# Kernel tuning notes

Measured on AMD Instinct MI355X. Metric: run time of the kernel, lower is better.

## Reference

```python
import jax, jax.numpy as jnp
import numpy as np

EMBED = 256; HEADS = 8; LEVELS = 1; POINTS = 4; QUEUE = 2
HB = 200; WB = 200; NQ = HB * WB; BS = 1


def bilinear_sample(img, grid, h, w):
    # img: (BH, D, h*w) flattened feature map; grid: (BH, N, 2) in [-1, 1]
    # torch.grid_sample(align_corners=False, padding_mode='zeros') semantics
    gx, gy = grid[..., 0], grid[..., 1]
    x = (gx + 1.0) * (w * 0.5) - 0.5
    y = (gy + 1.0) * (h * 0.5) - 0.5
    x0 = jnp.floor(x); y0 = jnp.floor(y)
    lx = x - x0; ly = y - y0
    x0i = x0.astype(jnp.int32); y0i = y0.astype(jnp.int32)

    def corner(xi, yi, wgt):
        valid = ((xi >= 0) & (xi < w) & (yi >= 0) & (yi < h)).astype(img.dtype)
        idx = jnp.clip(yi, 0, h - 1) * w + jnp.clip(xi, 0, w - 1)  # (BH, N)
        vals = jax.vmap(lambda im, ix: im[:, ix])(img, idx)  # (BH, D, N)
        return vals * (wgt * valid)[:, None, :]

    return (corner(x0i, y0i, (1 - lx) * (1 - ly))
            + corner(x0i + 1, y0i, lx * (1 - ly))
            + corner(x0i, y0i + 1, (1 - lx) * ly)
            + corner(x0i + 1, y0i + 1, lx * ly))


def ms_deform_attn(value, shapes, loc, aw):
    # value: (B, Nv, H, D); loc: (B, nq, H, L, P, 2); aw: (B, nq, H, L, P)
    B, Nv, H, D = value.shape
    nq = loc.shape[1]; P = loc.shape[4]
    grids = 2.0 * loc - 1.0
    start = 0
    per_level = []
    for l in range(shapes.shape[0]):
        h, w = int(shapes[l, 0]), int(shapes[l, 1])
        vl = value[:, start:start + h * w].reshape(B, h, w, H, D)
        vl = vl.transpose(0, 3, 4, 1, 2).reshape(B * H, D, h * w)
        g = grids[:, :, :, l].transpose(0, 2, 1, 3, 4).reshape(B * H, nq * P, 2)
        samp = bilinear_sample(vl, g, h, w).reshape(B, H, D, nq, P)
        per_level.append(samp)
        start += h * w
    sampled = jnp.stack(per_level, axis=4)  # (B, H, D, nq, L, P)
    w_ = aw.transpose(0, 2, 1, 3, 4)[:, :, None]  # (B, H, 1, nq, L, P)
    out = (sampled * w_).sum(axis=(-1, -2))  # (B, H, D, nq)
    return out.reshape(B, H * D, nq).transpose(0, 2, 1)  # (B, nq, E)


def setup_inputs():
    key = jax.random.key(0)
    ks = jax.random.split(key, 10)
    s = 0.02
    n_off = QUEUE * HEADS * LEVELS * POINTS * 2
    n_aw = QUEUE * HEADS * LEVELS * POINTS
    return {
        "query": jax.random.normal(ks[0], (BS, NQ, EMBED), jnp.float32),
        "query_pos": jax.random.normal(ks[1], (BS, NQ, EMBED), jnp.float32),
        "value": jax.random.normal(ks[2], (BS * QUEUE, NQ, EMBED), jnp.float32),
        "reference_points": jax.random.uniform(ks[3], (BS * QUEUE, NQ, LEVELS, 2), jnp.float32),
        "spatial_shapes": jnp.array([[HB, WB]], dtype=jnp.int32),
        "W_off": jax.random.normal(ks[4], (EMBED * QUEUE, n_off), jnp.float32) * s,
        "b_off": jnp.zeros((n_off,), jnp.float32),
        "W_attn": jax.random.normal(ks[5], (EMBED * QUEUE, n_aw), jnp.float32) * s,
        "b_attn": jnp.zeros((n_aw,), jnp.float32),
        "W_val": jax.random.normal(ks[6], (EMBED, EMBED), jnp.float32) * s,
        "b_val": jnp.zeros((EMBED,), jnp.float32),
        "W_out": jax.random.normal(ks[7], (EMBED, EMBED), jnp.float32) * s,
        "b_out": jnp.zeros((EMBED,), jnp.float32),
    }


def reference(query, query_pos, value, reference_points, spatial_shapes,
              W_off, b_off, W_attn, b_attn, W_val, b_val, W_out, b_out):
    shapes = np.asarray(spatial_shapes)  # static level shapes
    bs, nq, E = query.shape
    identity = query
    q = query + query_pos
    # temporal query: concat current-frame value with query
    q2 = jnp.concatenate([value[:bs], q], axis=-1)  # (bs, nq, 2E)
    v = value @ W_val + b_val  # (bs*2, nv, E)
    nv = v.shape[1]
    v = v.reshape(bs * QUEUE, nv, HEADS, E // HEADS)
    off = (q2 @ W_off + b_off).reshape(bs, nq, HEADS, QUEUE, LEVELS, POINTS, 2)
    aw = (q2 @ W_attn + b_attn).reshape(bs, nq, HEADS, QUEUE, LEVELS * POINTS)
    aw = jax.nn.softmax(aw, axis=-1).reshape(bs, nq, HEADS, QUEUE, LEVELS, POINTS)
    aw = aw.transpose(0, 3, 1, 2, 4, 5).reshape(bs * QUEUE, nq, HEADS, LEVELS, POINTS)
    off = off.transpose(0, 3, 1, 2, 4, 5, 6).reshape(bs * QUEUE, nq, HEADS, LEVELS, POINTS, 2)
    # normalized sampling locations: (bs*2, nq, H, L, P, 2)
    normalizer = jnp.stack([spatial_shapes[..., 1], spatial_shapes[..., 0]], -1).astype(jnp.float32)
    loc = reference_points[:, :, None, :, None, :] + off / normalizer[None, None, None, :, None, :]
    out = ms_deform_attn(v, shapes, loc, aw)  # (bs*2, nq, E)
    # average over the BEV queue (current + history)
    out = out.transpose(1, 2, 0).reshape(nq, E, bs, QUEUE).mean(-1).transpose(2, 0, 1)
    out = out @ W_out + b_out
    return out + identity
```

## Files before the change

### kernel.cpp

```cpp
#include <hip/hip_runtime.h>
#include <math.h>

#define NQ    40000
#define EMB   256
#define NHEAD 8
#define HDIM  32
#define HB    200
#define WB    200
#define NCOL  192

typedef __attribute__((ext_vector_type(8))) __bf16 bf16x8;
typedef __attribute__((ext_vector_type(4))) float f32x4;

static __device__ __forceinline__ unsigned short f2bf(float f) {
  unsigned u = __float_as_uint(f);
  u = u + 0x7fffu + ((u >> 16) & 1u);
  return (unsigned short)(u >> 16);
}
static __device__ __forceinline__ float bf2f(unsigned short s) {
  return __uint_as_float(((unsigned)s) << 16);
}

__global__ __launch_bounds__(256) void conv_w(
    const float* __restrict__ W_off, const float* __restrict__ b_off,
    const float* __restrict__ W_attn, const float* __restrict__ b_attn,
    const float* __restrict__ W_val, const float* __restrict__ W_out,
    unsigned short* __restrict__ Wc1t, unsigned short* __restrict__ Wvt,
    unsigned short* __restrict__ Wot, float* __restrict__ bc1)
{
  int idx = blockIdx.x * 256 + threadIdx.x;
  if (idx < 98304) {
    int n = idx >> 9, k = idx & 511;
    float v = (n < 128) ? W_off[(size_t)k * 128 + n] : W_attn[(size_t)k * 64 + (n - 128)];
    Wc1t[idx] = f2bf(v);
  } else if (idx < 163840) {
    int j = idx - 98304;
    int n = j >> 8, k = j & 255;
    Wvt[j] = f2bf(W_val[(size_t)k * 256 + n]);
  } else if (idx < 229376) {
    int j = idx - 163840;
    int n = j >> 8, k = j & 255;
    Wot[j] = f2bf(W_out[(size_t)k * 256 + n]);
  } else if (idx < 229568) {
    int n = idx - 229376;
    bc1[n] = (n < 128) ? b_off[n] : b_attn[n - 128];
  }
}

template<int K, int N, int AMODE, int OMODE, bool RESID>
__global__ __launch_bounds__(256, 4) void rb_gemm(
    const void* __restrict__ Aptr, const void* __restrict__ Aq2a,
    const void* __restrict__ Aq2b, const unsigned short* __restrict__ Bt,
    const float* __restrict__ bias, const float* __restrict__ resid,
    void* __restrict__ outp)
{
  constexpr int NFR = N / 64;
  constexpr int NP  = N + 8;
  constexpr int ATB = (AMODE != 0) ? 32 * K * 2 : 0;
  constexpr int TRB = (OMODE == 1) ? 32 * NP * 2 : 0;
  constexpr int MXB = (ATB > TRB) ? ATB : TRB;
  constexpr int LDSB = (MXB > 64) ? MXB : 64;
  __shared__ __align__(16) char lds[LDSB];
  unsigned short* trn = (unsigned short*)lds;

  const int t = threadIdx.x;
  const int m0 = blockIdx.x * 32;
  const int wid = t >> 6, lane = t & 63;
  const int wn = wid * (N / 4);
  const int lr = lane & 15, quad = lane >> 4;

  auto cvt_store = [&](int r, int c, float4 f0, float4 f1) {
    union { unsigned short us[8]; uint4 v; } u;
    u.us[0] = f2bf(f0.x); u.us[1] = f2bf(f0.y);
    u.us[2] = f2bf(f0.z); u.us[3] = f2bf(f0.w);
    u.us[4] = f2bf(f1.x); u.us[5] = f2bf(f1.y);
    u.us[6] = f2bf(f1.z); u.us[7] = f2bf(f1.w);
    *(uint4*)(lds + (size_t)r * (K * 2) + ((c ^ (r & 7)) * 16)) = u.v;
  };

  if constexpr (AMODE == 1) {
    const int c = t & 31, r0 = t >> 5;
    float4 f[4][2];
    #pragma unroll
    for (int l = 0; l < 4; l++) {
      const float* s = (const float*)Aptr + (size_t)(m0 + r0 + 8 * l) * K + c * 8;
      f[l][0] = *(const float4*)s; f[l][1] = *(const float4*)(s + 4);
    }
    #pragma unroll
    for (int l = 0; l < 4; l++)
      cvt_store(r0 + 8 * l, c, f[l][0], f[l][1]);
    __syncthreads();
  } else if constexpr (AMODE == 2) {
    const int c = t & 63, r0 = t >> 6;
    if (c < 32) {
      float4 f[8][2];
      #pragma unroll
      for (int l = 0; l < 8; l++) {
        const float* s = (const float*)Aptr + (size_t)(m0 + r0 + 4 * l) * 256 + c * 8;
        f[l][0] = *(const float4*)s; f[l][1] = *(const float4*)(s + 4);
      }
      #pragma unroll
      for (int l = 0; l < 8; l++)
        cvt_store(r0 + 4 * l, c, f[l][0], f[l][1]);
    } else {
      #pragma unroll
      for (int h = 0; h < 2; h++) {
        float4 fq[4][2], fp[4][2];
        #pragma unroll
        for (int l = 0; l < 4; l++) {
          int r = r0 + 4 * (h * 4 + l);
          const float* sq = (const float*)Aq2a + (size_t)(m0 + r) * 256 + (c - 32) * 8;
          const float* sp = (const float*)Aq2b + (size_t)(m0 + r) * 256 + (c - 32) * 8;
          fq[l][0] = *(const float4*)sq; fq[l][1] = *(const float4*)(sq + 4);
          fp[l][0] = *(const float4*)sp; fp[l][1] = *(const float4*)(sp + 4);
        }
        #pragma unroll
        for (int l = 0; l < 4; l++) {
          int r = r0 + 4 * (h * 4 + l);
          float4 f0 = make_float4(fq[l][0].x + fp[l][0].x, fq[l][0].y + fp[l][0].y,
                                  fq[l][0].z + fp[l][0].z, fq[l][0].w + fp[l][0].w);
          float4 f1 = make_float4(fq[l][1].x + fp[l][1].x, fq[l][1].y + fp[l][1].y,
                                  fq[l][1].z + fp[l][1].z, fq[l][1].w + fp[l][1].w);
          cvt_store(r, c, f0, f1);
        }
      }
    }
    __syncthreads();
  }

  f32x4 acc[2][NFR];
  #pragma unroll
  for (int i = 0; i < 2; i++)
    #pragma unroll
    for (int n = 0; n < NFR; n++) acc[i][n] = (f32x4){0.f, 0.f, 0.f, 0.f};

  auto loadB = [&](bf16x8* dst, int k0) {
    #pragma unroll
    for (int n = 0; n < NFR; n++)
      dst[n] = *(const bf16x8*)(Bt + (size_t)(wn + n * 16 + lr) * K + k0 + quad * 8);
  };
  auto loadA = [&](bf16x8* dst, int k0) {
    if constexpr (AMODE == 0) {
      const unsigned short* A = (const unsigned short*)Aptr;
      #pragma unroll
      for (int i = 0; i < 2; i++)
        dst[i] = *(const bf16x8*)(A + (size_t)(m0 + lr + i * 16) * K + k0 + quad * 8);
    } else {
      const int cb = (k0 >> 3) + quad;
      const int sw = (cb ^ (lr & 7)) * 16;
      #pragma unroll
      for (int i = 0; i < 2; i++)
        dst[i] = *(const bf16x8*)(lds + (size_t)(lr + i * 16) * (K * 2) + sw);
    }
  };

  constexpr int NK = K / 32;
  bf16x8 bcur[NFR], af[2];
  loadB(bcur, 0);
  loadA(af, 0);
  #pragma unroll
  for (int ks = 0; ks < NK; ks++) {
    bf16x8 bnxt[NFR], anxt[2];
    if (ks + 1 < NK) {
      loadB(bnxt, (ks + 1) * 32);
      loadA(anxt, (ks + 1) * 32);
    }
    #pragma unroll
    for (int i = 0; i < 2; i++)
      #pragma unroll
      for (int n = 0; n < NFR; n++)
        acc[i][n] = __builtin_amdgcn_mfma_f32_16x16x32_bf16(af[i], bcur[n], acc[i][n], 0, 0, 0);
    if (ks + 1 < NK) {
      #pragma unroll
      for (int n = 0; n < NFR; n++) bcur[n] = bnxt[n];
      af[0] = anxt[0]; af[1] = anxt[1];
    }
  }

  if constexpr (OMODE == 0) {
    #pragma unroll
    for (int i = 0; i < 2; i++) {
      int rowb = m0 + i * 16 + quad * 4;
      #pragma unroll
      for (int n = 0; n < NFR; n++) {
        int col = wn + n * 16 + lr;
        float bsv = bias[col];
        #pragma unroll
        for (int r = 0; r < 4; r++) {
          int rr = rowb + r;
          float v = acc[i][n][r] + bsv;
          if (RESID) v += resid[(size_t)rr * N + col];
          ((float*)outp)[(size_t)rr * N + col] = v;
        }
      }
    }
  } else {
    if constexpr (AMODE != 0) __syncthreads();
    #pragma unroll
    for (int i = 0; i < 2; i++) {
      #pragma unroll
      for (int n = 0; n < NFR; n++) {
        int col = wn + n * 16 + lr;
        float bsv = bias[col];
        #pragma unroll
        for (int r = 0; r < 4; r++) {
          int rl = i * 16 + quad * 4 + r;
          trn[rl * NP + col] = f2bf(acc[i][n][r] + bsv);
        }
      }
    }
    __syncthreads();
    constexpr int NCH = (32 * N) / 2048;
    #pragma unroll
    for (int l = 0; l < NCH; l++) {
      int c = t + l * 256;
      int row = c / (N / 8);
      int coloff = (c % (N / 8)) * 8;
      uint4 d = *(const uint4*)(trn + row * NP + coloff);
      *(uint4*)((unsigned short*)outp + (size_t)(m0 + row) * N + coloff) = d;
    }
  }
}

__global__ __launch_bounds__(256) void k3_sample(
    const unsigned short* __restrict__ raw1, const float* __restrict__ refp,
    const unsigned short* __restrict__ v, unsigned short* __restrict__ msd)
{
  __shared__ int4   sidx[2][64];
  __shared__ float4 swgt[2][64];
  const int t = threadIdx.x;
  const int q0 = blockIdx.x * 2;

  if (t < 128) {
    const int s = t >> 6, e = t & 63;
    const int b = e >> 5, h = (e >> 2) & 7, p = e & 3;
    const int q = q0 + s;
    const unsigned short* r = raw1 + (size_t)q * NCOL;
    float ox = bf2f(r[h * 16 + b * 8 + p * 2 + 0]);
    float oy = bf2f(r[h * 16 + b * 8 + p * 2 + 1]);
    float l0 = bf2f(r[128 + h * 8 + b * 4 + 0]);
    float l1 = bf2f(r[128 + h * 8 + b * 4 + 1]);
    float l2 = bf2f(r[128 + h * 8 + b * 4 + 2]);
    float l3 = bf2f(r[128 + h * 8 + b * 4 + 3]);
    float mx = fmaxf(fmaxf(l0, l1), fmaxf(l2, l3));
    float e0 = expf(l0 - mx), e1 = expf(l1 - mx);
    float e2 = expf(l2 - mx), e3 = expf(l3 - mx);
    float ssum = e0 + e1 + e2 + e3;
    float ep = (p == 0) ? e0 : (p == 1) ? e1 : (p == 2) ? e2 : e3;
    float aw = ep / ssum * 0.5f;
    float rx = refp[((size_t)b * NQ + q) * 2 + 0];
    float ry = refp[((size_t)b * NQ + q) * 2 + 1];
    float px = rx * (float)WB + ox - 0.5f;
    float py = ry * (float)HB + oy - 0.5f;
    float x0f = floorf(px), y0f = floorf(py);
    float lx = px - x0f, ly = py - y0f;
    int x0 = (int)x0f, y0 = (int)y0f, x1 = x0 + 1, y1 = y0 + 1;
    int x0c = min(max(x0, 0), WB - 1), x1c = min(max(x1, 0), WB - 1);
    int y0c = min(max(y0, 0), HB - 1), y1c = min(max(y1, 0), HB - 1);
    float vx0 = ((unsigned)x0 < (unsigned)WB) ? 1.f : 0.f;
    float vx1 = ((unsigned)x1 < (unsigned)WB) ? 1.f : 0.f;
    float vy0 = ((unsigned)y0 < (unsigned)HB) ? 1.f : 0.f;
    float vy1 = ((unsigned)y1 < (unsigned)HB) ? 1.f : 0.f;
    const int pb = b * NQ;
    const int hb = h * HDIM;
    int4 ix;
    ix.x = (pb + y0c * WB + x0c) * EMB + hb;
    ix.y = (pb + y0c * WB + x1c) * EMB + hb;
    ix.z = (pb + y1c * WB + x0c) * EMB + hb;
    ix.w = (pb + y1c * WB + x1c) * EMB + hb;
    float4 wv;
    wv.x = aw * (1.f - lx) * (1.f - ly) * vx0 * vy0;
    wv.y = aw * lx * (1.f - ly) * vx1 * vy0;
    wv.z = aw * (1.f - lx) * ly * vx0 * vy1;
    wv.w = aw * lx * ly * vx1 * vy1;
    sidx[s][e] = ix;
    swgt[s][e] = wv;
  }
  __syncthreads();

  const int s = t >> 7, u = t & 127;
  const int h = u >> 4, d2 = u & 15;
  const unsigned short* vd = v + d2 * 2;
  float a0 = 0.f, a1 = 0.f;
  #pragma unroll
  for (int b = 0; b < 2; b++) {
    #pragma unroll
    for (int p = 0; p < 4; p++) {
      int ent = b * 32 + h * 4 + p;
      int4 ix = sidx[s][ent];
      float4 wv = swgt[s][ent];
      unsigned c00 = *(const unsigned*)(vd + ix.x);
      unsigned c10 = *(const unsigned*)(vd + ix.y);
      unsigned c01 = *(const unsigned*)(vd + ix.z);
      unsigned c11 = *(const unsigned*)(vd + ix.w);
      a0 += wv.x * __uint_as_float(c00 << 16);
      a1 += wv.x * __uint_as_float(c00 & 0xffff0000u);
      a0 += wv.y * __uint_as_float(c10 << 16);
      a1 += wv.y * __uint_as_float(c10 & 0xffff0000u);
      a0 += wv.z * __uint_as_float(c01 << 16);
      a1 += wv.z * __uint_as_float(c01 & 0xffff0000u);
      a0 += wv.w * __uint_as_float(c11 << 16);
      a1 += wv.w * __uint_as_float(c11 & 0xffff0000u);
    }
  }
  unsigned pack = ((unsigned)f2bf(a1) << 16) | (unsigned)f2bf(a0);
  *(unsigned*)(msd + (size_t)(q0 + s) * EMB + h * HDIM + d2 * 2) = pack;
}

extern "C" void kernel_launch(void* const* d_in, const int* in_sizes, int n_in,
                              void* d_out, int out_size, void* d_ws, size_t ws_size,
                              hipStream_t stream) {
  const float* query     = (const float*)d_in[0];
  const float* query_pos = (const float*)d_in[1];
  const float* value     = (const float*)d_in[2];
  const float* refp      = (const float*)d_in[3];
  const float* W_off  = (const float*)d_in[5];
  const float* b_off  = (const float*)d_in[6];
  const float* W_attn = (const float*)d_in[7];
  const float* b_attn = (const float*)d_in[8];
  const float* W_val  = (const float*)d_in[9];
  const float* b_val  = (const float*)d_in[10];
  const float* W_out  = (const float*)d_in[11];
  const float* b_out  = (const float*)d_in[12];
  float* out = (float*)d_out;

  char* ws = (char*)d_ws;
  unsigned short* raw1 = (unsigned short*)(ws);
  unsigned short* vout = (unsigned short*)(ws + 15360000);
  unsigned short* msdb = (unsigned short*)(ws + 56320000);
  unsigned short* Wc1t = (unsigned short*)(ws + 76800000);
  unsigned short* Wvt  = (unsigned short*)(ws + 76996608);
  unsigned short* Wot  = (unsigned short*)(ws + 77127680);
  float*          bc1  = (float*)(ws + 77258752);

  hipLaunchKernelGGL(conv_w, dim3(897), dim3(256), 0, stream,
                     W_off, b_off, W_attn, b_attn, W_val, W_out, Wc1t, Wvt, Wot, bc1);

  hipLaunchKernelGGL((rb_gemm<512, 192, 2, 1, false>),
                     dim3(1250), dim3(256), 0, stream,
                     (const void*)value, (const void*)query, (const void*)query_pos,
                     Wc1t, bc1, (const float*)nullptr, (void*)raw1);
  hipLaunchKernelGGL((rb_gemm<256, 256, 1, 1, false>),
                     dim3(2500), dim3(256), 0, stream,
                     (const void*)value, (const void*)nullptr, (const void*)nullptr,
                     Wvt, b_val, (const float*)nullptr, (void*)vout);
  hipLaunchKernelGGL(k3_sample, dim3(NQ / 2), dim3(256), 0, stream,
                     raw1, refp, vout, msdb);
  hipLaunchKernelGGL((rb_gemm<256, 256, 0, 0, true>),
                     dim3(1250), dim3(256), 0, stream,
                     (const void*)msdb, (const void*)nullptr, (const void*)nullptr,
                     Wot, b_out, query, (void*)out);
}
```

Before: 366.4 us.

## Store value projection head-major and gather 16-byte vectors in sampler

The value-projection GEMM now writes its output in a head-major layout (head, pixel, 32 channels), so each head's 64-byte channel vector sits contiguously per pixel. The sampling kernel processes 8 queries per block, and each thread gathers a full uint4 of 8 bf16 channels per corner instead of 4-byte pairs. This cuts the number of gather instructions and improves per-request granularity. It costs more registers per thread (8 accumulators) and a strided output store in the GEMM epilogue.

```diff
diff --git a/kernel.cpp b/kernel.cpp
--- a/kernel.cpp
+++ b/kernel.cpp
@@ -8,6 +8,7 @@
 #define HB    200
 #define WB    200
 #define NCOL  192
+#define HPIX  2560000
 
 typedef __attribute__((ext_vector_type(8))) __bf16 bf16x8;
 typedef __attribute__((ext_vector_type(4))) float f32x4;
@@ -19,6 +20,16 @@
 }
 static __device__ __forceinline__ float bf2f(unsigned short s) {
   return __uint_as_float(((unsigned)s) << 16);
+}
+static __device__ __forceinline__ void acc8(float* a, uint4 u, float w) {
+  a[0] += w * __uint_as_float(u.x << 16);
+  a[1] += w * __uint_as_float(u.x & 0xffff0000u);
+  a[2] += w * __uint_as_float(u.y << 16);
+  a[3] += w * __uint_as_float(u.y & 0xffff0000u);
+  a[4] += w * __uint_as_float(u.z << 16);
+  a[5] += w * __uint_as_float(u.z & 0xffff0000u);
+  a[6] += w * __uint_as_float(u.w << 16);
+  a[7] += w * __uint_as_float(u.w & 0xffff0000u);
 }
 
 __global__ __launch_bounds__(256) void conv_w(
@@ -57,7 +68,7 @@
   constexpr int NFR = N / 64;
   constexpr int NP  = N + 8;
   constexpr int ATB = (AMODE != 0) ? 32 * K * 2 : 0;
-  constexpr int TRB = (OMODE == 1) ? 32 * NP * 2 : 0;
+  constexpr int TRB = (OMODE != 0) ? 32 * NP * 2 : 0;
   constexpr int MXB = (ATB > TRB) ? ATB : TRB;
   constexpr int LDSB = (MXB > 64) ? MXB : 64;
   __shared__ __align__(16) char lds[LDSB];
@@ -217,24 +228,31 @@
       int row = c / (N / 8);
       int coloff = (c % (N / 8)) * 8;
       uint4 d = *(const uint4*)(trn + row * NP + coloff);
-      *(uint4*)((unsigned short*)outp + (size_t)(m0 + row) * N + coloff) = d;
+      unsigned short* op = (unsigned short*)outp;
+      if constexpr (OMODE == 2)
+        op += (size_t)(coloff >> 5) * HPIX + (size_t)(m0 + row) * 32 + (coloff & 31);
+      else
+        op += (size_t)(m0 + row) * N + coloff;
+      *(uint4*)op = d;
     }
   }
 }
 
 __global__ __launch_bounds__(256) void k3_sample(
     const unsigned short* __restrict__ raw1, const float* __restrict__ refp,
-    const unsigned short* __restrict__ v, unsigned short* __restrict__ msd)
+    const unsigned short* __restrict__ vh, unsigned short* __restrict__ msd)
 {
-  __shared__ int4   sidx[2][64];
-  __shared__ float4 swgt[2][64];
+  __shared__ int4   sidx[8][64];
+  __shared__ float4 swgt[8][64];
   const int t = threadIdx.x;
-  const int q0 = blockIdx.x * 2;
-
-  if (t < 128) {
-    const int s = t >> 6, e = t & 63;
-    const int b = e >> 5, h = (e >> 2) & 7, p = e & 3;
-    const int q = q0 + s;
+  const int q0 = blockIdx.x * 8;
+
+  #pragma unroll
+  for (int ee = 0; ee < 2; ee++) {
+    const int e = t + ee * 256;
+    const int qi = e >> 6, r6 = e & 63;
+    const int b = r6 >> 5, h = (r6 >> 2) & 7, p = r6 & 3;
+    const int q = q0 + qi;
     const unsigned short* r = raw1 + (size_t)q * NCOL;
     float ox = bf2f(r[h * 16 + b * 8 + p * 2 + 0]);
     float oy = bf2f(r[h * 16 + b * 8 + p * 2 + 1]);
@@ -262,49 +280,47 @@
     float vy0 = ((unsigned)y0 < (unsigned)HB) ? 1.f : 0.f;
     float vy1 = ((unsigned)y1 < (unsigned)HB) ? 1.f : 0.f;
     const int pb = b * NQ;
-    const int hb = h * HDIM;
     int4 ix;
-    ix.x = (pb + y0c * WB + x0c) * EMB + hb;
-    ix.y = (pb + y0c * WB + x1c) * EMB + hb;
-    ix.z = (pb + y1c * WB + x0c) * EMB + hb;
-    ix.w = (pb + y1c * WB + x1c) * EMB + hb;
+    ix.x = pb + y0c * WB + x0c;
+    ix.y = pb + y0c * WB + x1c;
+    ix.z = pb + y1c * WB + x0c;
+    ix.w = pb + y1c * WB + x1c;
     float4 wv;
     wv.x = aw * (1.f - lx) * (1.f - ly) * vx0 * vy0;
     wv.y = aw * lx * (1.f - ly) * vx1 * vy0;
     wv.z = aw * (1.f - lx) * ly * vx0 * vy1;
     wv.w = aw * lx * ly * vx1 * vy1;
-    sidx[s][e] = ix;
-    swgt[s][e] = wv;
+    sidx[qi][r6] = ix;
+    swgt[qi][r6] = wv;
   }
   __syncthreads();
 
-  const int s = t >> 7, u = t & 127;
-  const int h = u >> 4, d2 = u & 15;
-  const unsigned short* vd = v + d2 * 2;
-  float a0 = 0.f, a1 = 0.f;
+  const int qi = t >> 5, h = (t >> 2) & 7, c = t & 3;
+  const unsigned short* vb = vh + (size_t)h * HPIX + c * 8;
+  float a[8];
+  #pragma unroll
+  for (int j = 0; j < 8; j++) a[j] = 0.f;
   #pragma unroll
   for (int b = 0; b < 2; b++) {
     #pragma unroll
     for (int p = 0; p < 4; p++) {
       int ent = b * 32 + h * 4 + p;
-      int4 ix = sidx[s][ent];
-      float4 wv = swgt[s][ent];
-      unsigned c00 = *(const unsigned*)(vd + ix.x);
-      unsigned c10 = *(const unsigned*)(vd + ix.y);
-      unsigned c01 = *(const unsigned*)(vd + ix.z);
-      unsigned c11 = *(const unsigned*)(vd + ix.w);
-      a0 += wv.x * __uint_as_float(c00 << 16);
-      a1 += wv.x * __uint_as_float(c00 & 0xffff0000u);
-      a0 += wv.y * __uint_as_float(c10 << 16);
-      a1 += wv.y * __uint_as_float(c10 & 0xffff0000u);
-      a0 += wv.z * __uint_as_float(c01 << 16);
-      a1 += wv.z * __uint_as_float(c01 & 0xffff0000u);
-      a0 += wv.w * __uint_as_float(c11 << 16);
-      a1 += wv.w * __uint_as_float(c11 & 0xffff0000u);
-    }
-  }
-  unsigned pack = ((unsigned)f2bf(a1) << 16) | (unsigned)f2bf(a0);
-  *(unsigned*)(msd + (size_t)(q0 + s) * EMB + h * HDIM + d2 * 2) = pack;
+      int4 pix = sidx[qi][ent];
+      float4 wv = swgt[qi][ent];
+      uint4 v00 = *(const uint4*)(vb + (size_t)pix.x * 32);
+      uint4 v10 = *(const uint4*)(vb + (size_t)pix.y * 32);
+      uint4 v01 = *(const uint4*)(vb + (size_t)pix.z * 32);
+      uint4 v11 = *(const uint4*)(vb + (size_t)pix.w * 32);
+      acc8(a, v00, wv.x);
+      acc8(a, v10, wv.y);
+      acc8(a, v01, wv.z);
+      acc8(a, v11, wv.w);
+    }
+  }
+  union { unsigned short us[8]; uint4 v; } o;
+  #pragma unroll
+  for (int j = 0; j < 8; j++) o.us[j] = f2bf(a[j]);
+  *(uint4*)(msd + (size_t)(q0 + qi) * EMB + h * HDIM + c * 8) = o.v;
 }
 
 extern "C" void kernel_launch(void* const* d_in, const int* in_sizes, int n_in,
@@ -340,11 +356,11 @@
                      dim3(1250), dim3(256), 0, stream,
                      (const void*)value, (const void*)query, (const void*)query_pos,
                      Wc1t, bc1, (const float*)nullptr, (void*)raw1);
-  hipLaunchKernelGGL((rb_gemm<256, 256, 1, 1, false>),
+  hipLaunchKernelGGL((rb_gemm<256, 256, 1, 2, false>),
                      dim3(2500), dim3(256), 0, stream,
                      (const void*)value, (const void*)nullptr, (const void*)nullptr,
                      Wvt, b_val, (const float*)nullptr, (void*)vout);
-  hipLaunchKernelGGL(k3_sample, dim3(NQ / 2), dim3(256), 0, stream,
+  hipLaunchKernelGGL(k3_sample, dim3(NQ / 8), dim3(256), 0, stream,
                      raw1, refp, vout, msdb);
   hipLaunchKernelGGL((rb_gemm<256, 256, 0, 0, true>),
                      dim3(1250), dim3(256), 0, stream,
```

Measured after the change: 373.0 us. About the same (+1.8%).
